# Optimization experiments

Measured on AMD Instinct MI355X. Metric: run time of the kernel, lower is better.

Reference implementation:

```python
import jax, jax.numpy as jnp
import numpy as np

B, N, D_IN, D_OUT, MAX_POS = 256, 256, 768, 300, 256
NEG_INF = -9e15
LEAKY_SLOPE = 0.2


def setup_inputs() -> dict:
    key = jax.random.key(0)
    ks = jax.random.split(key, 6)
    h = jax.random.normal(ks[0], (B, N, D_IN), dtype=jnp.float32)
    adj = (jax.random.uniform(ks[1], (B, N, N)) > 0.9).astype(jnp.float32)
    adj = jnp.maximum(adj, jnp.eye(N, dtype=jnp.float32)[None])
    positions = jax.random.randint(ks[2], (B, N), 0, MAX_POS)
    W = jax.random.normal(ks[3], (D_IN, D_OUT), dtype=jnp.float32) * (1.0 / np.sqrt(D_IN))
    a_src = jax.random.normal(ks[4], (1, D_OUT), dtype=jnp.float32) * 0.05
    a_dst = jax.random.normal(ks[5], (1, D_OUT), dtype=jnp.float32) * 0.05
    pos_table = jax.random.normal(jax.random.fold_in(key, 7), (MAX_POS, D_OUT), dtype=jnp.float32)
    return {"h": h, "adj": adj, "positions": positions, "W": W,
            "a_src": a_src, "a_dst": a_dst, "pos_table": pos_table}


def reference(h, adj, positions, W, a_src, a_dst, pos_table):
    # Wh = W(h) + position embedding          [B, N, D_OUT]
    Wh = jnp.einsum('bni,io->bno', h, W) + pos_table[positions]
    # additive attention scores
    f_src = jnp.einsum('bno,o->bn', Wh, a_src[0])  # [B, N]
    f_dst = jnp.einsum('bno,o->bn', Wh, a_dst[0])  # [B, N]
    e = f_src[:, :, None] + f_dst[:, None, :]      # [B, N, N]
    e = jnp.where(e >= 0, e, LEAKY_SLOPE * e)      # LeakyReLU(0.2)
    # adjacency masking + softmax over last dim
    masked = jnp.where(adj > 0, e, NEG_INF)
    attention = jax.nn.softmax(masked, axis=-1)
    # (eval mode: edge dropout and dropout are identity)
    h_prime = jnp.einsum('bnm,bmo->bno', attention, Wh)
    return h_prime, attention
```

## Files before the change

kernel.cpp:

```cpp
#include <hip/hip_runtime.h>

#define B_    256
#define N_    256
#define DIN   768
#define DOUT  300
#define DOUTP 320
#define M_    (B_*N_)
#define HP_ELEMS (M_*DOUT)
#define NEG_INF -9.0e15f

typedef _Float16 f16;
typedef __attribute__((ext_vector_type(8))) _Float16 f16x8;
typedef __attribute__((ext_vector_type(4))) _Float16 f16x4;
typedef __attribute__((ext_vector_type(4))) float    f32x4;

__device__ __forceinline__ void async_copy16(void* lds, const void* g) {
    __builtin_amdgcn_global_load_lds(
        (const __attribute__((address_space(1))) void*)g,
        (__attribute__((address_space(3))) void*)lds, 16, 0, 0);
}

__global__ __launch_bounds__(256) void prep_wt(const float* __restrict__ W,
                                               f16* __restrict__ Wt) {
    int idx = blockIdx.x * 256 + threadIdx.x;
    if (idx >= DOUTP * DIN) return;
    int n = idx / DIN, k = idx - n * DIN;
    float v = (n < DOUT) ? W[k * DOUT + n] : 0.0f;
    Wt[idx] = (f16)v;
}

__global__ __launch_bounds__(256, 2) void gemm1(
    const float* __restrict__ h, const f16* __restrict__ Wt,
    const int* __restrict__ positions,
    const float* __restrict__ a_src, const float* __restrict__ a_dst,
    const float* __restrict__ pos_table,
    f16* __restrict__ WhT, float* __restrict__ f_src, float* __restrict__ f_dst)
{
    __shared__ f16 Al[2][64 * 40];
    __shared__ f16 Bl[3][DOUTP * 32];
    __shared__ float pfs[64][2], pfd[64][2];

    const int tid  = threadIdx.x;
    const int wave = tid >> 6, lane = tid & 63;
    const int quad = lane >> 4, c = lane & 15;
    const int rh = wave & 1;
    const int chf = wave >> 1;
    const int rowbase = blockIdx.x * 64;

    const int brow = lane >> 2;
    const int bj   = (lane & 3) ^ (brow & 3);
    const int ar = tid >> 2, aj = tid & 3;

    const float* abase = h + (size_t)(rowbase + ar) * DIN + aj * 8;

    f32x4 acc[2][10];
#pragma unroll
    for (int rt = 0; rt < 2; ++rt)
#pragma unroll
        for (int i = 0; i < 10; ++i) acc[rt][i] = (f32x4){0.f, 0.f, 0.f, 0.f};

#define STAGE_B(K, BUF) do {                                                   \
    _Pragma("unroll")                                                          \
    for (int i_ = 0; i_ < 5; ++i_) {                                           \
        int chk_ = wave + 4 * i_;                                              \
        int n_ = chk_ * 16 + brow;                                             \
        async_copy16((char*)Bl[(BUF)] + chk_ * 1024,                           \
                     Wt + (size_t)n_ * DIN + (size_t)(K) * 32 + bj * 8);       \
    } } while (0)

#define LOAD_A(K, V0, V1) do {                                                 \
    const float4* s_ = (const float4*)(abase + (size_t)(K) * 32);              \
    V0 = s_[0]; V1 = s_[1]; } while (0)

#define WRITE_A(BUF, V0, V1)                                                   \
    *(f16x8*)&Al[(BUF)][ar * 40 + aj * 8] =                                    \
        (f16x8){(f16)V0.x, (f16)V0.y, (f16)V0.z, (f16)V0.w,                    \
                (f16)V1.x, (f16)V1.y, (f16)V1.z, (f16)V1.w}

    float4 r0a, r0b, r1a, r1b;

    STAGE_B(0, 0); LOAD_A(0, r0a, r0b);
    asm volatile("" ::: "memory");
    STAGE_B(1, 1); LOAD_A(1, r1a, r1b);
    WRITE_A(0, r0a, r0b);
    asm volatile("s_waitcnt vmcnt(7)" ::: "memory");
    asm volatile("s_waitcnt lgkmcnt(0)" ::: "memory");
    __builtin_amdgcn_s_barrier();
    asm volatile("" ::: "memory");

#define ITER(KT, CB, NB, CA, PF, WA, BAR) do {                                 \
    if (PF) {                                                                  \
        STAGE_B((KT) + 2, NB);                                                 \
        if ((CA) == 0) { LOAD_A((KT) + 2, r0a, r0b); }                         \
        else           { LOAD_A((KT) + 2, r1a, r1b); }                         \
    }                                                                          \
    {                                                                          \
        f16x8 af0 = *(const f16x8*)&Al[(CA)][(rh * 32 + c) * 40 + quad * 8];   \
        f16x8 af1 = *(const f16x8*)&Al[(CA)][(rh * 32 + 16 + c) * 40 + quad * 8]; \
        _Pragma("unroll")                                                      \
        for (int i_ = 0; i_ < 10; ++i_) {                                      \
            int n_ = (chf * 10 + i_) * 16 + c;                                 \
            f16x8 bf = *(const f16x8*)&Bl[(CB)][n_ * 32 + (quad ^ (n_ & 3)) * 8]; \
            acc[0][i_] = __builtin_amdgcn_mfma_f32_16x16x32_f16(af0, bf, acc[0][i_], 0, 0, 0); \
            acc[1][i_] = __builtin_amdgcn_mfma_f32_16x16x32_f16(af1, bf, acc[1][i_], 0, 0, 0); \
        }                                                                      \
    }                                                                          \
    if (WA) {                                                                  \
        if ((CA) == 0) { WRITE_A((CA) ^ 1, r1a, r1b); }                        \
        else           { WRITE_A((CA) ^ 1, r0a, r0b); }                        \
    }                                                                          \
    if (BAR) {                                                                 \
        if (PF) { asm volatile("s_waitcnt vmcnt(7)" ::: "memory"); }           \
        else    { asm volatile("s_waitcnt vmcnt(0)" ::: "memory"); }           \
        asm volatile("s_waitcnt lgkmcnt(0)" ::: "memory");                     \
        __builtin_amdgcn_s_barrier();                                          \
        asm volatile("" ::: "memory");                                         \
    }                                                                          \
} while (0)

    for (int kb = 0; kb < 18; kb += 6) {
        ITER(kb + 0, 0, 2, 0, 1, 1, 1);
        ITER(kb + 1, 1, 0, 1, 1, 1, 1);
        ITER(kb + 2, 2, 1, 0, 1, 1, 1);
        ITER(kb + 3, 0, 2, 1, 1, 1, 1);
        ITER(kb + 4, 1, 0, 0, 1, 1, 1);
        ITER(kb + 5, 2, 1, 1, 1, 1, 1);
    }
    ITER(18, 0, 2, 0, 1, 1, 1);
    ITER(19, 1, 0, 1, 1, 1, 1);
    ITER(20, 2, 1, 0, 1, 1, 1);
    ITER(21, 0, 2, 1, 1, 1, 1);
    ITER(22, 1, 0, 0, 0, 1, 1);
    ITER(23, 2, 1, 1, 0, 0, 0);

#undef ITER
#undef WRITE_A
#undef LOAD_A
#undef STAGE_B

    const int bidx  = rowbase >> 8;
    const int mloc  = (rowbase & 255);

    int posr[2][4];
#pragma unroll
    for (int rt = 0; rt < 2; ++rt)
#pragma unroll
        for (int r = 0; r < 4; ++r)
            posr[rt][r] = positions[rowbase + rh * 32 + rt * 16 + quad * 4 + r];

    float fs[2][4] = {{0,0,0,0},{0,0,0,0}}, fd[2][4] = {{0,0,0,0},{0,0,0,0}};
#pragma unroll
    for (int i = 0; i < 10; ++i) {
        int col = (chf * 10 + i) * 16 + c;
        if (col < DOUT) {
            float as = a_src[col], ad = a_dst[col];
#pragma unroll
            for (int rt = 0; rt < 2; ++rt)
#pragma unroll
                for (int r = 0; r < 4; ++r) {
                    float v = acc[rt][i][r] + pos_table[posr[rt][r] * DOUT + col];
                    acc[rt][i][r] = v;
                    fs[rt][r] += v * as;
                    fd[rt][r] += v * ad;
                }
        } else {
#pragma unroll
            for (int rt = 0; rt < 2; ++rt)
#pragma unroll
                for (int r = 0; r < 4; ++r) acc[rt][i][r] = 0.0f;
        }
    }
#pragma unroll
    for (int off = 1; off < 16; off <<= 1) {
#pragma unroll
        for (int rt = 0; rt < 2; ++rt)
#pragma unroll
            for (int r = 0; r < 4; ++r) {
                fs[rt][r] += __shfl_xor(fs[rt][r], off, 16);
                fd[rt][r] += __shfl_xor(fd[rt][r], off, 16);
            }
    }
    if (c == 0) {
#pragma unroll
        for (int rt = 0; rt < 2; ++rt)
#pragma unroll
            for (int r = 0; r < 4; ++r) {
                int row = rh * 32 + rt * 16 + quad * 4 + r;
                pfs[row][chf] = fs[rt][r];
                pfd[row][chf] = fd[rt][r];
            }
    }
#pragma unroll
    for (int i = 0; i < 10; ++i) {
        int col = (chf * 10 + i) * 16 + c;
#pragma unroll
        for (int rt = 0; rt < 2; ++rt) {
            int mrow = mloc + rh * 32 + rt * 16 + quad * 4;
            f16x4 u = (f16x4){(f16)acc[rt][i][0], (f16)acc[rt][i][1],
                              (f16)acc[rt][i][2], (f16)acc[rt][i][3]};
            *(f16x4*)(WhT + ((size_t)bidx * DOUTP + col) * N_ + mrow) = u;
        }
    }
    __syncthreads();
    if (tid < 64) {
        f_src[rowbase + tid] = pfs[tid][0] + pfs[tid][1];
        f_dst[rowbase + tid] = pfd[tid][0] + pfd[tid][1];
    }
}

__global__ __launch_bounds__(256, 2) void fused2(
    const float* __restrict__ adj, const float* __restrict__ f_src,
    const float* __restrict__ f_dst, const f16* __restrict__ WhT,
    float* __restrict__ att, float* __restrict__ hp)
{
    __shared__ f16 Pl[64 * 264];
    __shared__ f16 Bl[2][DOUTP * 32];

    const int tid  = threadIdx.x;
    const int wave = tid >> 6, lane = tid & 63;
    const int quad = lane >> 4, c = lane & 15;
    const int rh = wave & 1;
    const int chf = wave >> 1;
    const int rowbase = blockIdx.x * 64;
    const int bidx = rowbase >> 8;

    const int brow = lane >> 2;
    const int bj   = (lane & 3) ^ (brow & 3);

#define STAGE_B2(K, BUF) do {                                                  \
    _Pragma("unroll")                                                          \
    for (int i_ = 0; i_ < 5; ++i_) {                                           \
        int chk_ = wave + 4 * i_;                                              \
        int n_ = chk_ * 16 + brow;                                             \
        async_copy16((char*)Bl[(BUF)] + chk_ * 1024,                           \
                     WhT + ((size_t)bidx * DOUTP + n_) * N_ + (size_t)(K) * 32 + bj * 8); \
    } } while (0)

    STAGE_B2(0, 0);
    STAGE_B2(1, 1);

    {
        float4 fd4 = *(const float4*)(f_dst + bidx * N_ + lane * 4);
        const float* arow = adj + (size_t)(rowbase + wave * 16) * N_ + lane * 4;
        float4 nx = *(const float4*)arow;
        for (int rr = 0; rr < 16; ++rr) {
            float4 a4 = nx;
            if (rr < 15) nx = *(const float4*)(arow + (size_t)(rr + 1) * N_);
            const int lrow = wave * 16 + rr;
            const int row  = rowbase + lrow;
            float fs = f_src[row];

            float v, e0, e1, e2, e3;
            v = fs + fd4.x; v = v >= 0.f ? v : 0.2f * v; e0 = a4.x > 0.f ? v : NEG_INF;
            v = fs + fd4.y; v = v >= 0.f ? v : 0.2f * v; e1 = a4.y > 0.f ? v : NEG_INF;
            v = fs + fd4.z; v = v >= 0.f ? v : 0.2f * v; e2 = a4.z > 0.f ? v : NEG_INF;
            v = fs + fd4.w; v = v >= 0.f ? v : 0.2f * v; e3 = a4.w > 0.f ? v : NEG_INF;

            float mx = fmaxf(fmaxf(e0, e1), fmaxf(e2, e3));
#pragma unroll
            for (int off = 1; off < 64; off <<= 1) mx = fmaxf(mx, __shfl_xor(mx, off, 64));

            float p0 = __expf(e0 - mx), p1 = __expf(e1 - mx);
            float p2 = __expf(e2 - mx), p3 = __expf(e3 - mx);
            float s = p0 + p1 + p2 + p3;
#pragma unroll
            for (int off = 1; off < 64; off <<= 1) s += __shfl_xor(s, off, 64);

            float inv = 1.0f / s;
            *(float4*)(att + (size_t)row * N_ + lane * 4) =
                make_float4(p0 * inv, p1 * inv, p2 * inv, p3 * inv);
            *(f16x4*)&Pl[lrow * 264 + lane * 4] =
                (f16x4){(f16)(p0 * inv), (f16)(p1 * inv), (f16)(p2 * inv), (f16)(p3 * inv)};
        }
    }
    __syncthreads();

    f32x4 acc[2][10];
#pragma unroll
    for (int rt = 0; rt < 2; ++rt)
#pragma unroll
        for (int i = 0; i < 10; ++i) acc[rt][i] = (f32x4){0.f, 0.f, 0.f, 0.f};

#pragma unroll
    for (int kt = 0; kt < 8; ++kt) {
        f16x8 af0 = *(const f16x8*)&Pl[(rh * 32 + c) * 264 + kt * 32 + quad * 8];
        f16x8 af1 = *(const f16x8*)&Pl[(rh * 32 + 16 + c) * 264 + kt * 32 + quad * 8];
#pragma unroll
        for (int i = 0; i < 10; ++i) {
            int n = (chf * 10 + i) * 16 + c;
            f16x8 bf = *(const f16x8*)&Bl[kt & 1][n * 32 + (quad ^ (n & 3)) * 8];
            acc[0][i] = __builtin_amdgcn_mfma_f32_16x16x32_f16(af0, bf, acc[0][i], 0, 0, 0);
            acc[1][i] = __builtin_amdgcn_mfma_f32_16x16x32_f16(af1, bf, acc[1][i], 0, 0, 0);
        }
        if (kt < 7) {
            __syncthreads();
            if (kt + 2 < 8) STAGE_B2(kt + 2, kt & 1);
        }
    }
#undef STAGE_B2

#pragma unroll
    for (int i = 0; i < 10; ++i) {
        int col = (chf * 10 + i) * 16 + c;
        if (col < DOUT) {
#pragma unroll
            for (int rt = 0; rt < 2; ++rt) {
                int row0 = rowbase + rh * 32 + rt * 16 + quad * 4;
#pragma unroll
                for (int r = 0; r < 4; ++r)
                    hp[(size_t)(row0 + r) * DOUT + col] = acc[rt][i][r];
            }
        }
    }
}

extern "C" void kernel_launch(void* const* d_in, const int* in_sizes, int n_in,
                              void* d_out, int out_size, void* d_ws, size_t ws_size,
                              hipStream_t stream)
{
    const float* h         = (const float*)d_in[0];
    const float* adj       = (const float*)d_in[1];
    const int*   positions = (const int*)d_in[2];
    const float* W         = (const float*)d_in[3];
    const float* a_src     = (const float*)d_in[4];
    const float* a_dst     = (const float*)d_in[5];
    const float* pos_table = (const float*)d_in[6];

    float* hp  = (float*)d_out;
    float* att = hp + HP_ELEMS;

    f16*   Wt    = (f16*)d_ws;
    f16*   WhT   = Wt + (size_t)DOUTP * DIN;
    float* f_src = (float*)(WhT + (size_t)B_ * DOUTP * N_);
    float* f_dst = f_src + M_;

    hipLaunchKernelGGL(prep_wt, dim3((DOUTP * DIN + 255) / 256), dim3(256), 0, stream, W, Wt);
    hipLaunchKernelGGL(gemm1,   dim3(M_ / 64), dim3(256), 0, stream,
                       h, Wt, positions, a_src, a_dst, pos_table, WhT, f_src, f_dst);
    hipLaunchKernelGGL(fused2,  dim3(M_ / 64), dim3(256), 0, stream,
                       adj, f_src, f_dst, WhT, att, hp);
}
```

Baseline: 448.7 us.

## Split gemm1 output columns across two blocks with partial attention-score sums

gemm1 now splits the 320 output columns into two 160-column halves handled by separate blocks, doubling the grid. Each block writes partial f_src/f_dst sums, and fused2 adds the two halves. The split halves the B tile in LDS and the accumulator registers, which allows 3 blocks per CU, and the A prefetch goes one stage deeper. The LDS swizzle is also changed in both kernels. The cost is that each 64-row strip of h is read and converted to f16 twice, and the A-side work is duplicated.

```diff
diff --git a/kernel.cpp b/kernel.cpp
--- a/kernel.cpp
+++ b/kernel.cpp
@@ -5,6 +5,7 @@
 #define DIN   768
 #define DOUT  300
 #define DOUTP 320
+#define DOUTC 160
 #define M_    (B_*N_)
 #define HP_ELEMS (M_*DOUT)
 #define NEG_INF -9.0e15f
@@ -19,6 +20,9 @@
         (const __attribute__((address_space(1))) void*)g,
         (__attribute__((address_space(3))) void*)lds, 16, 0, 0);
 }
+
+#define STR_(x) #x
+#define STR(x) STR_(x)
 
 __global__ __launch_bounds__(256) void prep_wt(const float* __restrict__ W,
                                                f16* __restrict__ Wt) {
@@ -29,44 +33,48 @@
     Wt[idx] = (f16)v;
 }
 
-__global__ __launch_bounds__(256, 2) void gemm1(
+__global__ __launch_bounds__(256, 3) void gemm1(
     const float* __restrict__ h, const f16* __restrict__ Wt,
     const int* __restrict__ positions,
     const float* __restrict__ a_src, const float* __restrict__ a_dst,
     const float* __restrict__ pos_table,
-    f16* __restrict__ WhT, float* __restrict__ f_src, float* __restrict__ f_dst)
+    f16* __restrict__ WhT, float* __restrict__ f_srcP, float* __restrict__ f_dstP)
 {
     __shared__ f16 Al[2][64 * 40];
-    __shared__ f16 Bl[3][DOUTP * 32];
+    __shared__ f16 Bl[3][DOUTC * 32];
     __shared__ float pfs[64][2], pfd[64][2];
 
     const int tid  = threadIdx.x;
     const int wave = tid >> 6, lane = tid & 63;
     const int quad = lane >> 4, c = lane & 15;
-    const int rh = wave & 1;
+    const int rh  = wave & 1;
     const int chf = wave >> 1;
-    const int rowbase = blockIdx.x * 64;
+    const int strip = blockIdx.x & 1023;
+    const int cs    = blockIdx.x >> 10;
+    const int rowbase = strip * 64;
+    const int colbase = cs * DOUTC;
 
     const int brow = lane >> 2;
-    const int bj   = (lane & 3) ^ (brow & 3);
+    const int bj   = (lane & 3) ^ ((lane >> 3) & 3);
     const int ar = tid >> 2, aj = tid & 3;
 
     const float* abase = h + (size_t)(rowbase + ar) * DIN + aj * 8;
 
-    f32x4 acc[2][10];
+    f32x4 acc[2][5];
 #pragma unroll
     for (int rt = 0; rt < 2; ++rt)
 #pragma unroll
-        for (int i = 0; i < 10; ++i) acc[rt][i] = (f32x4){0.f, 0.f, 0.f, 0.f};
+        for (int i = 0; i < 5; ++i) acc[rt][i] = (f32x4){0.f, 0.f, 0.f, 0.f};
 
 #define STAGE_B(K, BUF) do {                                                   \
-    _Pragma("unroll")                                                          \
-    for (int i_ = 0; i_ < 5; ++i_) {                                           \
-        int chk_ = wave + 4 * i_;                                              \
-        int n_ = chk_ * 16 + brow;                                             \
-        async_copy16((char*)Bl[(BUF)] + chk_ * 1024,                           \
-                     Wt + (size_t)n_ * DIN + (size_t)(K) * 32 + bj * 8);       \
-    } } while (0)
+    async_copy16((char*)Bl[(BUF)] + wave * 1024,                               \
+        Wt + (size_t)(colbase + wave * 16 + brow) * DIN + (size_t)(K) * 32 + bj * 8); \
+    async_copy16((char*)Bl[(BUF)] + (wave + 4) * 1024,                         \
+        Wt + (size_t)(colbase + (wave + 4) * 16 + brow) * DIN + (size_t)(K) * 32 + bj * 8); \
+    if (wave < 2)                                                              \
+        async_copy16((char*)Bl[(BUF)] + (wave + 8) * 1024,                     \
+            Wt + (size_t)(colbase + (wave + 8) * 16 + brow) * DIN + (size_t)(K) * 32 + bj * 8); \
+} while (0)
 
 #define LOAD_A(K, V0, V1) do {                                                 \
     const float4* s_ = (const float4*)(abase + (size_t)(K) * 32);              \
@@ -77,63 +85,61 @@
         (f16x8){(f16)V0.x, (f16)V0.y, (f16)V0.z, (f16)V0.w,                    \
                 (f16)V1.x, (f16)V1.y, (f16)V1.z, (f16)V1.w}
 
-    float4 r0a, r0b, r1a, r1b;
-
-    STAGE_B(0, 0); LOAD_A(0, r0a, r0b);
+#define COMPUTE(CB, CA) do {                                                   \
+    f16x8 af0 = *(const f16x8*)&Al[(CA)][(rh * 32 + c) * 40 + quad * 8];       \
+    f16x8 af1 = *(const f16x8*)&Al[(CA)][(rh * 32 + 16 + c) * 40 + quad * 8];  \
+    _Pragma("unroll")                                                          \
+    for (int i_ = 0; i_ < 5; ++i_) {                                           \
+        int nl_ = (chf * 5 + i_) * 16 + c;                                     \
+        f16x8 bf = *(const f16x8*)&Bl[(CB)][nl_ * 32 + (quad ^ ((nl_ >> 1) & 3)) * 8]; \
+        acc[0][i_] = __builtin_amdgcn_mfma_f32_16x16x32_f16(af0, bf, acc[0][i_], 0, 0, 0); \
+        acc[1][i_] = __builtin_amdgcn_mfma_f32_16x16x32_f16(af1, bf, acc[1][i_], 0, 0, 0); \
+    } } while (0)
+
+#define VMCNT_W(HI, LO) do {                                                   \
+    if (wave < 2) { asm volatile("s_waitcnt vmcnt(" STR(HI) ")" ::: "memory"); } \
+    else          { asm volatile("s_waitcnt vmcnt(" STR(LO) ")" ::: "memory"); } \
+} while (0)
+
+#define ITER(KT, CB, NB, CA, PFB, PFA, LV0, LV1, WA, WV0, WV1, BAR, VH, VL) do { \
+    if (PFB) { STAGE_B((KT) + 2, NB); }                                        \
+    if (PFA) { LOAD_A((KT) + 3, LV0, LV1); }                                   \
+    COMPUTE(CB, CA);                                                           \
+    if (WA)  { WRITE_A((CA) ^ 1, WV0, WV1); }                                  \
+    if (BAR) { VMCNT_W(VH, VL);                                                \
+               asm volatile("s_waitcnt lgkmcnt(0)" ::: "memory");              \
+               __builtin_amdgcn_s_barrier();                                   \
+               asm volatile("" ::: "memory"); }                                \
+} while (0)
+
+    float4 s0a, s0b, s1a, s1b, s2a, s2b;
+
+    STAGE_B(0, 0); LOAD_A(0, s0a, s0b);
     asm volatile("" ::: "memory");
-    STAGE_B(1, 1); LOAD_A(1, r1a, r1b);
-    WRITE_A(0, r0a, r0b);
-    asm volatile("s_waitcnt vmcnt(7)" ::: "memory");
+    STAGE_B(1, 1); LOAD_A(1, s1a, s1b); LOAD_A(2, s2a, s2b);
+    WRITE_A(0, s0a, s0b);
     asm volatile("s_waitcnt lgkmcnt(0)" ::: "memory");
     __builtin_amdgcn_s_barrier();
     asm volatile("" ::: "memory");
 
-#define ITER(KT, CB, NB, CA, PF, WA, BAR) do {                                 \
-    if (PF) {                                                                  \
-        STAGE_B((KT) + 2, NB);                                                 \
-        if ((CA) == 0) { LOAD_A((KT) + 2, r0a, r0b); }                         \
-        else           { LOAD_A((KT) + 2, r1a, r1b); }                         \
-    }                                                                          \
-    {                                                                          \
-        f16x8 af0 = *(const f16x8*)&Al[(CA)][(rh * 32 + c) * 40 + quad * 8];   \
-        f16x8 af1 = *(const f16x8*)&Al[(CA)][(rh * 32 + 16 + c) * 40 + quad * 8]; \
-        _Pragma("unroll")                                                      \
-        for (int i_ = 0; i_ < 10; ++i_) {                                      \
-            int n_ = (chf * 10 + i_) * 16 + c;                                 \
-            f16x8 bf = *(const f16x8*)&Bl[(CB)][n_ * 32 + (quad ^ (n_ & 3)) * 8]; \
-            acc[0][i_] = __builtin_amdgcn_mfma_f32_16x16x32_f16(af0, bf, acc[0][i_], 0, 0, 0); \
-            acc[1][i_] = __builtin_amdgcn_mfma_f32_16x16x32_f16(af1, bf, acc[1][i_], 0, 0, 0); \
-        }                                                                      \
-    }                                                                          \
-    if (WA) {                                                                  \
-        if ((CA) == 0) { WRITE_A((CA) ^ 1, r1a, r1b); }                        \
-        else           { WRITE_A((CA) ^ 1, r0a, r0b); }                        \
-    }                                                                          \
-    if (BAR) {                                                                 \
-        if (PF) { asm volatile("s_waitcnt vmcnt(7)" ::: "memory"); }           \
-        else    { asm volatile("s_waitcnt vmcnt(0)" ::: "memory"); }           \
-        asm volatile("s_waitcnt lgkmcnt(0)" ::: "memory");                     \
-        __builtin_amdgcn_s_barrier();                                          \
-        asm volatile("" ::: "memory");                                         \
-    }                                                                          \
-} while (0)
-
-    for (int kb = 0; kb < 18; kb += 6) {
-        ITER(kb + 0, 0, 2, 0, 1, 1, 1);
-        ITER(kb + 1, 1, 0, 1, 1, 1, 1);
-        ITER(kb + 2, 2, 1, 0, 1, 1, 1);
-        ITER(kb + 3, 0, 2, 1, 1, 1, 1);
-        ITER(kb + 4, 1, 0, 0, 1, 1, 1);
-        ITER(kb + 5, 2, 1, 1, 1, 1, 1);
-    }
-    ITER(18, 0, 2, 0, 1, 1, 1);
-    ITER(19, 1, 0, 1, 1, 1, 1);
-    ITER(20, 2, 1, 0, 1, 1, 1);
-    ITER(21, 0, 2, 1, 1, 1, 1);
-    ITER(22, 1, 0, 0, 0, 1, 1);
-    ITER(23, 2, 1, 1, 0, 0, 0);
+    ITER(0, 0, 2, 0, 1, 1, s0a, s0b, 1, s1a, s1b, 1, 9, 8);
+    for (int kb = 1; kb < 19; kb += 6) {
+        ITER(kb + 0, 1, 0, 1, 1, 1, s1a, s1b, 1, s2a, s2b, 1, 7, 6);
+        ITER(kb + 1, 2, 1, 0, 1, 1, s2a, s2b, 1, s0a, s0b, 1, 7, 6);
+        ITER(kb + 2, 0, 2, 1, 1, 1, s0a, s0b, 1, s1a, s1b, 1, 7, 6);
+        ITER(kb + 3, 1, 0, 0, 1, 1, s1a, s1b, 1, s2a, s2b, 1, 7, 6);
+        ITER(kb + 4, 2, 1, 1, 1, 1, s2a, s2b, 1, s0a, s0b, 1, 7, 6);
+        ITER(kb + 5, 0, 2, 0, 1, 1, s0a, s0b, 1, s1a, s1b, 1, 7, 6);
+    }
+    ITER(19, 1, 0, 1, 1, 1, s1a, s1b, 1, s2a, s2b, 1, 7, 6);
+    ITER(20, 2, 1, 0, 1, 1, s2a, s2b, 1, s0a, s0b, 1, 7, 6);
+    ITER(21, 0, 2, 1, 1, 0, s0a, s0b, 1, s1a, s1b, 1, 5, 4);
+    ITER(22, 1, 0, 0, 0, 0, s0a, s0b, 1, s2a, s2b, 1, 0, 0);
+    ITER(23, 2, 0, 1, 0, 0, s0a, s0b, 0, s0a, s0b, 0, 0, 0);
 
 #undef ITER
+#undef VMCNT_W
+#undef COMPUTE
 #undef WRITE_A
 #undef LOAD_A
 #undef STAGE_B
@@ -150,8 +156,8 @@
 
     float fs[2][4] = {{0,0,0,0},{0,0,0,0}}, fd[2][4] = {{0,0,0,0},{0,0,0,0}};
 #pragma unroll
-    for (int i = 0; i < 10; ++i) {
-        int col = (chf * 10 + i) * 16 + c;
+    for (int i = 0; i < 5; ++i) {
+        int col = colbase + (chf * 5 + i) * 16 + c;
         if (col < DOUT) {
             float as = a_src[col], ad = a_dst[col];
 #pragma unroll
@@ -191,8 +197,8 @@
             }
     }
 #pragma unroll
-    for (int i = 0; i < 10; ++i) {
-        int col = (chf * 10 + i) * 16 + c;
+    for (int i = 0; i < 5; ++i) {
+        int col = colbase + (chf * 5 + i) * 16 + c;
 #pragma unroll
         for (int rt = 0; rt < 2; ++rt) {
             int mrow = mloc + rh * 32 + rt * 16 + quad * 4;
@@ -203,14 +209,14 @@
     }
     __syncthreads();
     if (tid < 64) {
-        f_src[rowbase + tid] = pfs[tid][0] + pfs[tid][1];
-        f_dst[rowbase + tid] = pfd[tid][0] + pfd[tid][1];
+        f_srcP[(size_t)cs * M_ + rowbase + tid] = pfs[tid][0] + pfs[tid][1];
+        f_dstP[(size_t)cs * M_ + rowbase + tid] = pfd[tid][0] + pfd[tid][1];
     }
 }
 
 __global__ __launch_bounds__(256, 2) void fused2(
-    const float* __restrict__ adj, const float* __restrict__ f_src,
-    const float* __restrict__ f_dst, const f16* __restrict__ WhT,
+    const float* __restrict__ adj, const float* __restrict__ f_srcP,
+    const float* __restrict__ f_dstP, const f16* __restrict__ WhT,
     float* __restrict__ att, float* __restrict__ hp)
 {
     __shared__ f16 Pl[64 * 264];
@@ -225,7 +231,7 @@
     const int bidx = rowbase >> 8;
 
     const int brow = lane >> 2;
-    const int bj   = (lane & 3) ^ (brow & 3);
+    const int bj   = (lane & 3) ^ ((lane >> 3) & 3);
 
 #define STAGE_B2(K, BUF) do {                                                  \
     _Pragma("unroll")                                                          \
@@ -240,15 +246,20 @@
     STAGE_B2(1, 1);
 
     {
-        float4 fd4 = *(const float4*)(f_dst + bidx * N_ + lane * 4);
+        float4 fdA = *(const float4*)(f_dstP + bidx * N_ + lane * 4);
+        float4 fdB = *(const float4*)(f_dstP + M_ + bidx * N_ + lane * 4);
+        float4 fd4 = make_float4(fdA.x + fdB.x, fdA.y + fdB.y,
+                                 fdA.z + fdB.z, fdA.w + fdB.w);
         const float* arow = adj + (size_t)(rowbase + wave * 16) * N_ + lane * 4;
-        float4 nx = *(const float4*)arow;
+        float4 nx0 = *(const float4*)arow;
+        float4 nx1 = *(const float4*)(arow + N_);
         for (int rr = 0; rr < 16; ++rr) {
-            float4 a4 = nx;
-            if (rr < 15) nx = *(const float4*)(arow + (size_t)(rr + 1) * N_);
+            float4 a4 = nx0;
+            nx0 = nx1;
+            if (rr + 2 < 16) nx1 = *(const float4*)(arow + (size_t)(rr + 2) * N_);
             const int lrow = wave * 16 + rr;
             const int row  = rowbase + lrow;
-            float fs = f_src[row];
+            float fs = f_srcP[row] + f_srcP[M_ + row];
 
             float v, e0, e1, e2, e3;
             v = fs + fd4.x; v = v >= 0.f ? v : 0.2f * v; e0 = a4.x > 0.f ? v : NEG_INF;
@@ -288,7 +299,7 @@
 #pragma unroll
         for (int i = 0; i < 10; ++i) {
             int n = (chf * 10 + i) * 16 + c;
-            f16x8 bf = *(const f16x8*)&Bl[kt & 1][n * 32 + (quad ^ (n & 3)) * 8];
+            f16x8 bf = *(const f16x8*)&Bl[kt & 1][n * 32 + (quad ^ ((n >> 1) & 3)) * 8];
             acc[0][i] = __builtin_amdgcn_mfma_f32_16x16x32_f16(af0, bf, acc[0][i], 0, 0, 0);
             acc[1][i] = __builtin_amdgcn_mfma_f32_16x16x32_f16(af1, bf, acc[1][i], 0, 0, 0);
         }
@@ -329,14 +340,14 @@
     float* hp  = (float*)d_out;
     float* att = hp + HP_ELEMS;
 
-    f16*   Wt    = (f16*)d_ws;
-    f16*   WhT   = Wt + (size_t)DOUTP * DIN;
-    float* f_src = (float*)(WhT + (size_t)B_ * DOUTP * N_);
-    float* f_dst = f_src + M_;
+    f16*   Wt     = (f16*)d_ws;
+    f16*   WhT    = Wt + (size_t)DOUTP * DIN;
+    float* f_srcP = (float*)(WhT + (size_t)B_ * DOUTP * N_);
+    float* f_dstP = f_srcP + 2 * (size_t)M_;
 
     hipLaunchKernelGGL(prep_wt, dim3((DOUTP * DIN + 255) / 256), dim3(256), 0, stream, W, Wt);
-    hipLaunchKernelGGL(gemm1,   dim3(M_ / 64), dim3(256), 0, stream,
-                       h, Wt, positions, a_src, a_dst, pos_table, WhT, f_src, f_dst);
+    hipLaunchKernelGGL(gemm1,   dim3(2 * M_ / 64), dim3(256), 0, stream,
+                       h, Wt, positions, a_src, a_dst, pos_table, WhT, f_srcP, f_dstP);
     hipLaunchKernelGGL(fused2,  dim3(M_ / 64), dim3(256), 0, stream,
-                       adj, f_src, f_dst, WhT, att, hp);
-}
+                       adj, f_srcP, f_dstP, WhT, att, hp);
+}
```

Measured after the change: 479.2 us. 6.8% more time.
